# Performance work log

Measured on AMD Instinct MI355X. Metric: run time of the kernel, lower is better.

The kernel has to match this reference:

```python
import jax, jax.numpy as jnp
import numpy as np

H, W = 128, 192          # image size (height, width) after imsz swap
K = 31                   # weight_sl (local window size)
T = K // 2               # replicate padding
C_FEAT = 64              # feat_dim
FFT_ROWS, FFT_COLS = 32, 48  # rect fft mask (after '48,32' swap)


def fft_rect(x):
    # rfft2 low-pass rectangular mask, exactly as fft_ifft with 'rect'.
    f = jnp.fft.rfft2(x)
    rows = jnp.arange(f.shape[-2])[:, None] < FFT_ROWS
    cols = jnp.arange(f.shape[-1])[None, :] < FFT_COLS
    f = f * (rows & cols)
    return jnp.fft.irfft2(f, s=x.shape[-2:])


def make_grid():
    t = float(T)  # weight_sl//2 with downsample_factor=1
    xs = jnp.linspace(-t, t, K)
    gx, gy = jnp.meshgrid(xs, xs, indexing='ij')
    return jnp.stack((gx, gy), axis=-1)  # [K,K,2]


def local_corr(src, tgt):
    # src, tgt: [C,H,W] -> cost volume [H,W,K,K]
    sp = jnp.pad(src, ((0, 0), (T, T), (T, T)), mode='edge')  # replicate pad
    rows = []
    for k in range(K):  # fixed structural loop over window rows
        sl = sp[:, k:k + H, :]  # [C,H,W+2T]
        win = jax.lax.conv_general_dilated_patches(sl[None], (1, K), (1, 1), 'VALID')[0]
        win = win.reshape(C_FEAT, K, H, W)  # [C,l,H,W]
        rows.append(jnp.einsum('chw,clhw->hwl', tgt, win))
    return jnp.stack(rows, axis=-2)  # [H,W,k,l]


def setup_inputs() -> dict:
    key = jax.random.key(0)
    k1, k2, k3 = jax.random.split(key, 3)
    fill_val = (1.0 / C_FEAT) ** 0.5
    feats = fill_val + 0.02 * jax.random.normal(k1, (1, 2, C_FEAT, H, W), jnp.float32)
    in_frames = jax.random.normal(k2, (1, 1, 3, H, W), jnp.float32)
    tgt_frames = jax.random.normal(k3, (1, 1, 3, H, W), jnp.float32)
    return {"in_frames": in_frames, "tgt_frames": tgt_frames, "feats": feats, "temp": 10}


def reference(in_frames, tgt_frames, feats, temp):
    # src_idx=0, tgt_idx=1, single-frame 'feats' path
    src = fft_rect(feats[0, 0])  # [C,H,W]
    tgt = fft_rect(feats[0, 1])
    # bilinear interpolate(scale_factor=1) is identity
    src = src / jnp.linalg.norm(src, axis=0, keepdims=True)
    tgt = tgt / jnp.linalg.norm(tgt, axis=0, keepdims=True)
    w = local_corr(src, tgt) * temp                       # [H,W,K,K]
    w = jax.nn.softmax(w.reshape(H, W, K * K), axis=-1).reshape(H, W, K, K)

    # windowed average of in_frames with per-pixel softmax weights
    xp = jnp.pad(in_frames[0, 0], ((0, 0), (T, T), (T, T)), mode='edge')
    patches = jax.lax.conv_general_dilated_patches(xp[None], (K, K), (1, 1), 'VALID')[0]
    patches = patches.reshape(3, K, K, H, W)              # [C,k,l,H,W]
    out = jnp.einsum('cklhw,hwkl->chw', patches, w)[None, None]  # [1,1,3,H,W]

    grid = make_grid()                                    # [K,K,2]
    pos = jnp.einsum('hwkl,klm->hwm', w, grid)[None, None]
    pos = pos[..., ::-1]                                  # .flip(-1)
    enorm = jnp.einsum('hwkl,kl->hw', w, jnp.linalg.norm(grid, axis=-1))[None, None]
    weights = w[None, None]                               # [1,1,H,W,K,K]
    return out, pos, enorm, weights
```

## Files before the change

kernel.cpp:

```cpp
#include <hip/hip_runtime.h>
#include <cstddef>

#define H 128
#define W 192
#define KS 31
#define CF 64
#define NPIX (H*W)
#define NKL (KS*KS)

#define OFF_POS (3*NPIX)
#define OFF_EN  (OFF_POS + 2*NPIX)
#define OFF_WGT (OFF_EN + NPIX)

#define NIMG NPIX
#define WS_CWT 0
#define WS_SWT 512
#define WS_CHT 1024
#define WS_SHT 1536
#define WS_U   2048
#define WS_V   (WS_U + 128*NIMG)
#define WS_Y   (WS_V + 128*NIMG)
#define WS_SN  (WS_Y + 128*NIMG)
#define WS_TN  (WS_SN + 32*NIMG)

#define PI_F 3.14159265358979323846f

typedef __attribute__((ext_vector_type(8))) short short8v;
typedef __attribute__((ext_vector_type(4))) float f32x4;

__device__ inline ushort bf16rtn(float f){
  uint u = __float_as_uint(f);
  u += 0x7fffu + ((u >> 16) & 1u);
  return (ushort)(u >> 16);
}

__global__ __launch_bounds__(256) void k_tables(float* ws){
  int t = blockIdx.x*256 + threadIdx.x;
  if (t < 383){
    int d = t - 191;
    float c = 1.0f, s = 0.0f;
    for (int v = 1; v < 48; ++v){
      int m = (v*d) % 192; if (m < 0) m += 192;
      float a = (2.0f*PI_F/192.0f)*(float)m;
      c += 2.0f*cosf(a);
      s += 2.0f*sinf(a);
    }
    ws[WS_CWT + t] = c * (1.0f/192.0f);
    ws[WS_SWT + t] = s * (1.0f/192.0f);
  } else if (t < 383 + 255){
    int i = t - 383;
    int d = i - 127;
    float c = 0.0f, s = 0.0f;
    for (int u = 0; u < 32; ++u){
      int m = (u*d) % 128; if (m < 0) m += 128;
      float a = (2.0f*PI_F/128.0f)*(float)m;
      c += cosf(a);
      s += sinf(a);
    }
    ws[WS_CHT + i] = c * (1.0f/128.0f);
    ws[WS_SHT + i] = s * (1.0f/128.0f);
  }
}

__global__ __launch_bounds__(192) void k_colpass(const float* __restrict__ feats,
                                                const float* __restrict__ ws,
                                                float* __restrict__ U,
                                                float* __restrict__ V){
  __shared__ float xs[16][192];
  __shared__ float scw[384], ssw[384];
  int w  = threadIdx.x;
  int R0 = blockIdx.x * 16;
  for (int i = w; i < 383; i += 192){
    scw[i] = ws[WS_CWT + i];
    ssw[i] = ws[WS_SWT + i];
  }
#pragma unroll
  for (int r = 0; r < 16; ++r) xs[r][w] = feats[(size_t)(R0 + r)*192 + w];
  __syncthreads();
  float u[16], v[16];
#pragma unroll
  for (int r = 0; r < 16; ++r){ u[r] = 0.0f; v[r] = 0.0f; }
#pragma unroll 2
  for (int wp = 0; wp < 192; ++wp){
    float cw = scw[w - wp + 191];
    float sw = ssw[w - wp + 191];
#pragma unroll
    for (int r = 0; r < 16; ++r){
      float x = xs[r][wp];
      u[r] = fmaf(x, cw, u[r]);
      v[r] = fmaf(x, sw, v[r]);
    }
  }
#pragma unroll
  for (int r = 0; r < 16; ++r){
    U[(size_t)(R0 + r)*192 + w] = u[r];
    V[(size_t)(R0 + r)*192 + w] = v[r];
  }
}

__global__ __launch_bounds__(192) void k_rowpass(const float* __restrict__ U,
                                                const float* __restrict__ V,
                                                const float* __restrict__ ws,
                                                float* __restrict__ Y){
  __shared__ float scht[255], ssht[255];
  int w = threadIdx.x;
  for (int i = w; i < 255; i += 192){
    scht[i] = ws[WS_CHT + i];
    ssht[i] = ws[WS_SHT + i];
  }
  __syncthreads();
  int ch = blockIdx.x >> 3;
  int h0 = (blockIdx.x & 7) * 16;
  const float* Uc = U + (size_t)ch*NIMG;
  const float* Vc = V + (size_t)ch*NIMG;
  float acc[16];
#pragma unroll
  for (int r = 0; r < 16; ++r) acc[r] = 0.0f;
  for (int hp = 0; hp < 128; ++hp){
    float uu = Uc[hp*192 + w];
    float vv = Vc[hp*192 + w];
#pragma unroll
    for (int r = 0; r < 16; ++r){
      int idx = h0 + r - hp + 127;
      acc[r] = fmaf(uu,  scht[idx], acc[r]);
      acc[r] = fmaf(-vv, ssht[idx], acc[r]);
    }
  }
  for (int r = 0; r < 16; ++r)
    Y[(size_t)ch*NIMG + (h0 + r)*192 + w] = acc[r];
}

__global__ __launch_bounds__(192) void k_norm(const float* __restrict__ Y,
                                              ushort* __restrict__ SNh,
                                              ushort* __restrict__ TNh){
  int h = blockIdx.x, w = threadIdx.x;
  int which = blockIdx.y;
  int pix = h*192 + w;
  const float* base = Y + (size_t)which*64*NIMG + pix;
  float x[64];
  float ss = 0.0f;
#pragma unroll
  for (int c = 0; c < 64; ++c){
    x[c] = base[(size_t)c*NIMG];
    ss = fmaf(x[c], x[c], ss);
  }
  float rn = 1.0f / sqrtf(ss);
  ushort* o = (which ? TNh : SNh) + (size_t)pix*64;
#pragma unroll
  for (int q = 0; q < 8; ++q){
    ushort tmp[8];
#pragma unroll
    for (int e = 0; e < 8; ++e) tmp[e] = bf16rtn(x[q*8 + e] * rn);
    *reinterpret_cast<uint4*>(o + q*8) = *reinterpret_cast<const uint4*>(tmp);
  }
}

__global__ __launch_bounds__(256) void k_corrsm(const ushort* __restrict__ SNh,
                                                const ushort* __restrict__ TNh,
                                                const int* __restrict__ temp,
                                                const float* __restrict__ frames,
                                                float* __restrict__ dout){
  __shared__ float eL[16][993];
  __shared__ float red7[7][16][16];
  __shared__ float rsw[16];
  int h  = blockIdx.x;
  int bx = blockIdx.y;
  int t  = threadIdx.x;
  int lane = t & 63, wv = t >> 6;
  int n = lane & 15, g = lane >> 4;
  int w0 = bx * 16;
  float tempf = (float)(*temp);

  const ushort* ap = TNh + ((size_t)(h*192 + w0 + n))*64 + g*8;
  short8v a0 = *reinterpret_cast<const short8v*>(ap);
  short8v a1 = *reinterpret_cast<const short8v*>(ap + 32);

  for (int k = wv; k < KS; k += 4){
    int sh = h + k - 15; sh = sh < 0 ? 0 : (sh > 127 ? 127 : sh);
    const ushort* srow = SNh + (size_t)sh*192*64;
#pragma unroll
    for (int dj = 0; dj < 3; ++dj){
      int j0 = bx - 1 + dj;
      if (j0 < 0 || j0 > 11) continue;
      const ushort* bp = srow + ((size_t)(j0*16 + n))*64 + g*8;
      short8v b0 = *reinterpret_cast<const short8v*>(bp);
      short8v b1 = *reinterpret_cast<const short8v*>(bp + 32);
      f32x4 acc = {0.0f, 0.0f, 0.0f, 0.0f};
      acc = __builtin_amdgcn_mfma_f32_16x16x32_bf16(a0, b0, acc, 0, 0, 0);
      acc = __builtin_amdgcn_mfma_f32_16x16x32_bf16(a1, b1, acc, 0, 0, 0);
      int sx = j0*16 + n;
#pragma unroll
      for (int r = 0; r < 4; ++r){
        int wl = g*4 + r;
        int wg = w0 + wl;
        int l = sx - wg + 15;
        float e = __expf(acc[r]*tempf - tempf);
        if (l >= 0 && l <= 30) eL[wl][k*31 + l] = e;
        if (bx == 0 && j0 == 0 && n == 0){
          for (int l2 = 0; l2 < 15 - wg; ++l2) eL[wl][k*31 + l2] = e;
        }
        if (bx == 11 && j0 == 11 && n == 15){
          for (int l2 = 207 - wg; l2 <= 30; ++l2) eL[wl][k*31 + l2] = e;
        }
      }
    }
  }
  __syncthreads();

  {
    float s=0, o0=0, o1=0, o2=0, p0=0, p1=0, en=0;
    int wl = t & 15;
    int wg = w0 + wl;
    for (int kk = t >> 4; kk < KS; kk += 16){
      int sh = h + kk - 15; sh = sh < 0 ? 0 : (sh > 127 ? 127 : sh);
      float dy = (float)(kk - 15);
      float dy2 = dy*dy;
      const float* f0p = frames + sh*192;
      const float* f1p = f0p + NPIX;
      const float* f2p = f0p + 2*NPIX;
      const float* src = eL[wl] + kk*31;
#pragma unroll
      for (int l = 0; l < KS; ++l){
        float e = src[l];
        float dx = (float)(l - 15);
        int ww = wg + l - 15; ww = ww < 0 ? 0 : (ww > 191 ? 191 : ww);
        s  += e;
        p0 = fmaf(e, dx, p0);
        p1 = fmaf(e, dy, p1);
        en = fmaf(e, sqrtf(dx*dx + dy2), en);
        o0 = fmaf(e, f0p[ww], o0);
        o1 = fmaf(e, f1p[ww], o1);
        o2 = fmaf(e, f2p[ww], o2);
      }
    }
    int q = t >> 4;
    red7[0][q][wl]=s;  red7[1][q][wl]=o0; red7[2][q][wl]=o1; red7[3][q][wl]=o2;
    red7[4][q][wl]=p0; red7[5][q][wl]=p1; red7[6][q][wl]=en;
  }
  __syncthreads();

  if (t < 16){
    float a[7];
#pragma unroll
    for (int j = 0; j < 7; ++j){
      float acc = 0.0f;
#pragma unroll
      for (int qq = 0; qq < 16; ++qq) acc += red7[j][qq][t];
      a[j] = acc;
    }
    float rs = 1.0f / a[0];
    int pix = h*192 + w0 + t;
    dout[0*NPIX + pix] = a[1]*rs;
    dout[1*NPIX + pix] = a[2]*rs;
    dout[2*NPIX + pix] = a[3]*rs;
    dout[OFF_POS + pix*2 + 0] = a[4]*rs;
    dout[OFF_POS + pix*2 + 1] = a[5]*rs;
    dout[OFF_EN + pix] = a[6]*rs;
    rsw[t] = rs;
  }
  __syncthreads();

  {
    int w2 = t >> 4, q2 = t & 15;
    float rs = rsw[w2];
    float* dst = dout + OFF_WGT + ((size_t)(h*192 + w0 + w2))*NKL;
    const float* src = eL[w2];
    for (int j = q2; j < NKL; j += 16)
      dst[j] = src[j] * rs;
  }
}

extern "C" void kernel_launch(void* const* d_in, const int* in_sizes, int n_in,
                              void* d_out, int out_size, void* d_ws, size_t ws_size,
                              hipStream_t stream) {
  const float* frames = (const float*)d_in[0];
  const float* feats  = (const float*)d_in[2];
  const int*   temp   = (const int*)d_in[3];
  float* ws   = (float*)d_ws;
  float* dout = (float*)d_out;
  (void)in_sizes; (void)n_in; (void)out_size; (void)ws_size;

  float*  U   = ws + WS_U;
  float*  V   = ws + WS_V;
  float*  Y   = ws + WS_Y;
  ushort* SNh = (ushort*)(ws + WS_SN);
  ushort* TNh = (ushort*)(ws + WS_TN);

  hipLaunchKernelGGL(k_tables,  dim3(3),        dim3(256), 0, stream, ws);
  hipLaunchKernelGGL(k_colpass, dim3(1024),     dim3(192), 0, stream, feats, ws, U, V);
  hipLaunchKernelGGL(k_rowpass, dim3(1024),     dim3(192), 0, stream, U, V, ws, Y);
  hipLaunchKernelGGL(k_norm,    dim3(128, 2),   dim3(192), 0, stream, Y, SNh, TNh);
  hipLaunchKernelGGL(k_corrsm,  dim3(128, 12),  dim3(256), 0, stream, SNh, TNh, temp, frames, dout);
}
```

Baseline: 326.5 us.

## Vectorise DFT passes with shifted tables, interleave U/V, store softmax weights as bf16

The column and row DFT passes now read their twiddle tables as float4 from four pre-shifted shared-memory copies and read the feature rows four at a time. U and V are interleaved into one float2 buffer so each row-pass load fetches both. The correlation kernel stores exp values as bf16 in shared memory, which roughly halves LDS use and adds a minimum of 4 blocks per CU to launch bounds to raise occupancy. The weight write-back is reorganised so each wavefront writes whole rows. The exp values stored as bf16 lose precision, which affects both the accumulated sums and the written weights.

```diff
diff --git a/kernel.cpp b/kernel.cpp
--- a/kernel.cpp
+++ b/kernel.cpp
@@ -18,12 +18,12 @@
 #define WS_CHT 1024
 #define WS_SHT 1536
 #define WS_U   2048
-#define WS_V   (WS_U + 128*NIMG)
-#define WS_Y   (WS_V + 128*NIMG)
+#define WS_Y   (WS_U + 2*128*NIMG)
 #define WS_SN  (WS_Y + 128*NIMG)
 #define WS_TN  (WS_SN + 32*NIMG)
 
 #define PI_F 3.14159265358979323846f
+#define ELS 962
 
 typedef __attribute__((ext_vector_type(8))) short short8v;
 typedef __attribute__((ext_vector_type(4))) float f32x4;
@@ -33,6 +33,7 @@
   u += 0x7fffu + ((u >> 16) & 1u);
   return (ushort)(u >> 16);
 }
+__device__ inline float bf2f(ushort h){ return __uint_as_float((uint)h << 16); }
 
 __global__ __launch_bounds__(256) void k_tables(float* ws){
   int t = blockIdx.x*256 + threadIdx.x;
@@ -64,68 +65,95 @@
 
 __global__ __launch_bounds__(192) void k_colpass(const float* __restrict__ feats,
                                                 const float* __restrict__ ws,
-                                                float* __restrict__ U,
-                                                float* __restrict__ V){
+                                                float2* __restrict__ UV2){
   __shared__ float xs[16][192];
-  __shared__ float scw[384], ssw[384];
+  __shared__ float tc[4][392], tn[4][392];
   int w  = threadIdx.x;
   int R0 = blockIdx.x * 16;
-  for (int i = w; i < 383; i += 192){
-    scw[i] = ws[WS_CWT + i];
-    ssw[i] = ws[WS_SWT + i];
+  for (int i = w; i < 380; i += 192){
+#pragma unroll
+    for (int s = 0; s < 4; ++s){
+      tc[s][i] = ws[WS_CWT + i + s];
+      tn[s][i] = ws[WS_SWT + i + s];
+    }
   }
 #pragma unroll
   for (int r = 0; r < 16; ++r) xs[r][w] = feats[(size_t)(R0 + r)*192 + w];
   __syncthreads();
+
+  const int s = w & 3;
+  const int boff = (w & ~3) + 188;
+  const float* tcs = tc[s];
+  const float* tns = tn[s];
+
   float u[16], v[16];
 #pragma unroll
   for (int r = 0; r < 16; ++r){ u[r] = 0.0f; v[r] = 0.0f; }
-#pragma unroll 2
-  for (int wp = 0; wp < 192; ++wp){
-    float cw = scw[w - wp + 191];
-    float sw = ssw[w - wp + 191];
+
+  for (int wp0 = 0; wp0 < 192; wp0 += 4){
+    const float4 cw4 = *reinterpret_cast<const float4*>(tcs + (boff - wp0));
+    const float4 sw4 = *reinterpret_cast<const float4*>(tns + (boff - wp0));
 #pragma unroll
     for (int r = 0; r < 16; ++r){
-      float x = xs[r][wp];
-      u[r] = fmaf(x, cw, u[r]);
-      v[r] = fmaf(x, sw, v[r]);
-    }
-  }
-#pragma unroll
-  for (int r = 0; r < 16; ++r){
-    U[(size_t)(R0 + r)*192 + w] = u[r];
-    V[(size_t)(R0 + r)*192 + w] = v[r];
-  }
-}
-
-__global__ __launch_bounds__(192) void k_rowpass(const float* __restrict__ U,
-                                                const float* __restrict__ V,
+      const float4 x4 = *reinterpret_cast<const float4*>(&xs[r][wp0]);
+      u[r] = fmaf(x4.x, cw4.w, u[r]);
+      u[r] = fmaf(x4.y, cw4.z, u[r]);
+      u[r] = fmaf(x4.z, cw4.y, u[r]);
+      u[r] = fmaf(x4.w, cw4.x, u[r]);
+      v[r] = fmaf(x4.x, sw4.w, v[r]);
+      v[r] = fmaf(x4.y, sw4.z, v[r]);
+      v[r] = fmaf(x4.z, sw4.y, v[r]);
+      v[r] = fmaf(x4.w, sw4.x, v[r]);
+    }
+  }
+#pragma unroll
+  for (int r = 0; r < 16; ++r)
+    UV2[(size_t)(R0 + r)*192 + w] = make_float2(u[r], v[r]);
+}
+
+__global__ __launch_bounds__(192) void k_rowpass(const float2* __restrict__ UV2,
                                                 const float* __restrict__ ws,
                                                 float* __restrict__ Y){
-  __shared__ float scht[255], ssht[255];
+  __shared__ float Lc[4][144], Ls[4][144];
   int w = threadIdx.x;
-  for (int i = w; i < 255; i += 192){
-    scht[i] = ws[WS_CHT + i];
-    ssht[i] = ws[WS_SHT + i];
-  }
-  __syncthreads();
   int ch = blockIdx.x >> 3;
   int h0 = (blockIdx.x & 7) * 16;
-  const float* Uc = U + (size_t)ch*NIMG;
-  const float* Vc = V + (size_t)ch*NIMG;
+  for (int i = w; i < 143; i += 192){
+#pragma unroll
+    for (int s = 0; s < 4; ++s){
+      int gi = h0 + i + s;
+      Lc[s][i] = (gi < 255) ?  ws[WS_CHT + gi] : 0.0f;
+      Ls[s][i] = (gi < 255) ? -ws[WS_SHT + gi] : 0.0f;
+    }
+  }
+  __syncthreads();
+  const float2* Uc = UV2 + (size_t)ch*NIMG;
+
   float acc[16];
 #pragma unroll
   for (int r = 0; r < 16; ++r) acc[r] = 0.0f;
-  for (int hp = 0; hp < 128; ++hp){
-    float uu = Uc[hp*192 + w];
-    float vv = Vc[hp*192 + w];
+
+  for (int hp0 = 0; hp0 < 128; hp0 += 4){
+    float2 uv0 = Uc[(hp0+0)*192 + w];
+    float2 uv1 = Uc[(hp0+1)*192 + w];
+    float2 uv2 = Uc[(hp0+2)*192 + w];
+    float2 uv3 = Uc[(hp0+3)*192 + w];
 #pragma unroll
     for (int r = 0; r < 16; ++r){
-      int idx = h0 + r - hp + 127;
-      acc[r] = fmaf(uu,  scht[idx], acc[r]);
-      acc[r] = fmaf(-vv, ssht[idx], acc[r]);
-    }
-  }
+      int lb = 124 + (r & ~3) - hp0;
+      const float4 c4 = *reinterpret_cast<const float4*>(&Lc[r & 3][lb]);
+      const float4 s4 = *reinterpret_cast<const float4*>(&Ls[r & 3][lb]);
+      acc[r] = fmaf(uv0.x, c4.w, acc[r]);
+      acc[r] = fmaf(uv0.y, s4.w, acc[r]);
+      acc[r] = fmaf(uv1.x, c4.z, acc[r]);
+      acc[r] = fmaf(uv1.y, s4.z, acc[r]);
+      acc[r] = fmaf(uv2.x, c4.y, acc[r]);
+      acc[r] = fmaf(uv2.y, s4.y, acc[r]);
+      acc[r] = fmaf(uv3.x, c4.x, acc[r]);
+      acc[r] = fmaf(uv3.y, s4.x, acc[r]);
+    }
+  }
+#pragma unroll
   for (int r = 0; r < 16; ++r)
     Y[(size_t)ch*NIMG + (h0 + r)*192 + w] = acc[r];
 }
@@ -155,12 +183,12 @@
   }
 }
 
-__global__ __launch_bounds__(256) void k_corrsm(const ushort* __restrict__ SNh,
-                                                const ushort* __restrict__ TNh,
-                                                const int* __restrict__ temp,
-                                                const float* __restrict__ frames,
-                                                float* __restrict__ dout){
-  __shared__ float eL[16][993];
+__global__ __launch_bounds__(256, 4) void k_corrsm(const ushort* __restrict__ SNh,
+                                                   const ushort* __restrict__ TNh,
+                                                   const int* __restrict__ temp,
+                                                   const float* __restrict__ frames,
+                                                   float* __restrict__ dout){
+  __shared__ ushort eLu[16*ELS];
   __shared__ float red7[7][16][16];
   __shared__ float rsw[16];
   int h  = blockIdx.x;
@@ -195,12 +223,13 @@
         int wg = w0 + wl;
         int l = sx - wg + 15;
         float e = __expf(acc[r]*tempf - tempf);
-        if (l >= 0 && l <= 30) eL[wl][k*31 + l] = e;
+        ushort eb = bf16rtn(e);
+        if (l >= 0 && l <= 30) eLu[wl*ELS + k*31 + l] = eb;
         if (bx == 0 && j0 == 0 && n == 0){
-          for (int l2 = 0; l2 < 15 - wg; ++l2) eL[wl][k*31 + l2] = e;
+          for (int l2 = 0; l2 < 15 - wg; ++l2) eLu[wl*ELS + k*31 + l2] = eb;
         }
         if (bx == 11 && j0 == 11 && n == 15){
-          for (int l2 = 207 - wg; l2 <= 30; ++l2) eL[wl][k*31 + l2] = e;
+          for (int l2 = 207 - wg; l2 <= 30; ++l2) eLu[wl*ELS + k*31 + l2] = eb;
         }
       }
     }
@@ -218,10 +247,10 @@
       const float* f0p = frames + sh*192;
       const float* f1p = f0p + NPIX;
       const float* f2p = f0p + 2*NPIX;
-      const float* src = eL[wl] + kk*31;
+      const ushort* src = eLu + wl*ELS + kk*31;
 #pragma unroll
       for (int l = 0; l < KS; ++l){
-        float e = src[l];
+        float e = bf2f(src[l]);
         float dx = (float)(l - 15);
         int ww = wg + l - 15; ww = ww < 0 ? 0 : (ww > 191 ? 191 : ww);
         s  += e;
@@ -260,13 +289,18 @@
   }
   __syncthreads();
 
-  {
-    int w2 = t >> 4, q2 = t & 15;
-    float rs = rsw[w2];
-    float* dst = dout + OFF_WGT + ((size_t)(h*192 + w0 + w2))*NKL;
-    const float* src = eL[w2];
-    for (int j = q2; j < NKL; j += 16)
-      dst[j] = src[j] * rs;
+#pragma unroll
+  for (int rr = 0; rr < 4; ++rr){
+    int row = wv*4 + rr;
+    float rsv = rsw[row];
+    float* dst = dout + OFF_WGT + ((size_t)(h*192 + w0 + row))*NKL;
+    const ushort* src = eLu + row*ELS;
+#pragma unroll
+    for (int i = 0; i < 15; ++i){
+      int j = i*64 + lane;
+      dst[j] = bf2f(src[j]) * rsv;
+    }
+    if (lane == 0) dst[960] = bf2f(src[960]) * rsv;
   }
 }
 
@@ -280,15 +314,14 @@
   float* dout = (float*)d_out;
   (void)in_sizes; (void)n_in; (void)out_size; (void)ws_size;
 
-  float*  U   = ws + WS_U;
-  float*  V   = ws + WS_V;
+  float2* UV2 = (float2*)(ws + WS_U);
   float*  Y   = ws + WS_Y;
   ushort* SNh = (ushort*)(ws + WS_SN);
   ushort* TNh = (ushort*)(ws + WS_TN);
 
   hipLaunchKernelGGL(k_tables,  dim3(3),        dim3(256), 0, stream, ws);
-  hipLaunchKernelGGL(k_colpass, dim3(1024),     dim3(192), 0, stream, feats, ws, U, V);
-  hipLaunchKernelGGL(k_rowpass, dim3(1024),     dim3(192), 0, stream, U, V, ws, Y);
+  hipLaunchKernelGGL(k_colpass, dim3(1024),     dim3(192), 0, stream, feats, ws, UV2);
+  hipLaunchKernelGGL(k_rowpass, dim3(1024),     dim3(192), 0, stream, UV2, ws, Y);
   hipLaunchKernelGGL(k_norm,    dim3(128, 2),   dim3(192), 0, stream, Y, SNh, TNh);
   hipLaunchKernelGGL(k_corrsm,  dim3(128, 12),  dim3(256), 0, stream, SNh, TNh, temp, frames, dout);
 }
```

Result: faster. 307.3 us (-5.9%).
